# Optimization experiments

Hardware: AMD Instinct MI355X
Metric: run time of the kernel (lower is better)

The kernel has to match this reference:

```python
import jax, jax.numpy as jnp
import numpy as np
import math

B, S, IN, D, H, L, DFF = 8, 512, 32, 512, 8, 6, 2048
DK = D // H
LN_EPS = 1e-5
KL_EPS = 1e-8


def _pos_encoding(seq_len, d_model):
    pe = np.zeros((seq_len, d_model), dtype=np.float32)
    pos = np.arange(seq_len, dtype=np.float32)[:, None]
    div = np.exp(np.arange(0, d_model, 2, dtype=np.float32) * (-math.log(10000.0) / d_model))
    pe[:, 0::2] = np.sin(pos * div)
    pe[:, 1::2] = np.cos(pos * div)
    return jnp.asarray(pe)


def setup_inputs() -> dict:
    key = jax.random.key(0)
    ks = iter(jax.random.split(key, 32))
    g = lambda shape: jax.random.normal(next(ks), shape, dtype=jnp.float32) * 0.02
    return {
        'x': jax.random.normal(next(ks), (B, S, IN), dtype=jnp.float32),
        'W_in': g((IN, D)), 'b_in': jnp.zeros((D,), jnp.float32),
        'pe': _pos_encoding(S, D),
        'Wq': g((L, D, D)), 'Wk': g((L, D, D)), 'Wv': g((L, D, D)),
        'Wo': g((L, D, D)), 'bo': jnp.zeros((L, D), jnp.float32),
        'W1': g((L, D, DFF)), 'b1': jnp.zeros((L, DFF), jnp.float32),
        'W2': g((L, DFF, D)), 'b2': jnp.zeros((L, D), jnp.float32),
        'ln1_g': jnp.ones((L, D), jnp.float32), 'ln1_b': jnp.zeros((L, D), jnp.float32),
        'ln2_g': jnp.ones((L, D), jnp.float32), 'ln2_b': jnp.zeros((L, D), jnp.float32),
        'W_out': g((D, IN)), 'b_out': jnp.zeros((IN,), jnp.float32),
        'Ws1': g((D, D // 2)), 'bs1': jnp.zeros((D // 2,), jnp.float32),
        'Ws2': g((D // 2, 1)), 'bs2': jnp.zeros((1,), jnp.float32),
    }


def _layernorm(v, gamma, beta):
    mu = v.mean(-1, keepdims=True)
    var = ((v - mu) ** 2).mean(-1, keepdims=True)
    return (v - mu) * jax.lax.rsqrt(var + LN_EPS) * gamma + beta


def reference(x, W_in, b_in, pe, Wq, Wk, Wv, Wo, bo, W1, b1, W2, b2,
              ln1_g, ln1_b, ln2_g, ln2_b, W_out, b_out, Ws1, bs1, Ws2, bs2):
    b, s, _ = x.shape
    h = x @ W_in + b_in + pe[None, :s, :]
    total_assoc = jnp.zeros((b, s), x.dtype)
    scale = 1.0 / math.sqrt(DK)
    prior = 1.0 / s + KL_EPS
    for l in range(L):
        # QKV: [b, h, s, dk]
        Q = (h @ Wq[l]).reshape(b, s, H, DK).transpose(0, 2, 1, 3)
        K = (h @ Wk[l]).reshape(b, s, H, DK).transpose(0, 2, 1, 3)
        V = (h @ Wv[l]).reshape(b, s, H, DK).transpose(0, 2, 1, 3)
        scores = jnp.einsum('bhsk,bhtk->bhst', Q, K) * scale
        attn = jax.nn.softmax(scores, axis=-1)  # [b,h,s,s]
        ctx = jnp.einsum('bhst,bhtk->bhsk', attn, V)
        ctx = ctx.transpose(0, 2, 1, 3).reshape(b, s, D)
        attn_out = ctx @ Wo[l] + bo[l]
        # association discrepancy: KL(avg_attn || uniform prior) per query
        avg_attn = attn.mean(axis=1) + KL_EPS  # [b,s,s]
        total_assoc = total_assoc + (avg_attn * jnp.log(avg_attn / prior)).sum(-1)
        h = _layernorm(h + attn_out, ln1_g[l], ln1_b[l])
        ff = jax.nn.relu(h @ W1[l] + b1[l]) @ W2[l] + b2[l]
        h = _layernorm(h + ff, ln2_g[l], ln2_b[l])
    reconstruction = h @ W_out + b_out
    anomaly_scores = jax.nn.sigmoid(jax.nn.relu(h @ Ws1 + bs1) @ Ws2 + bs2)[..., 0]
    avg_association = total_assoc / L
    return reconstruction, anomaly_scores, avg_association
```

## Files before the change

kernel.cpp:

```cpp
#include <hip/hip_runtime.h>
#include <math.h>

typedef __attribute__((ext_vector_type(8))) short bf16x8;
typedef __attribute__((ext_vector_type(4))) float f32x4;

__device__ __forceinline__ short f2bf(float v) {
  union { float f; unsigned u; } x; x.f = v;
  unsigned r = x.u + 0x7fffu + ((x.u >> 16) & 1u);
  return (short)(r >> 16);
}

__device__ __forceinline__ float bf2f(unsigned short u) {
  union { unsigned u; float f; } x; x.u = ((unsigned)u) << 16;
  return x.f;
}

__device__ __forceinline__ void gld_lds16(const void* g, void* l) {
  __builtin_amdgcn_global_load_lds((const __attribute__((address_space(1))) void*)g,
                                   (__attribute__((address_space(3))) void*)l, 16, 0, 0);
}

__global__ __launch_bounds__(256) void transpose_bf(const float* __restrict__ src,
                                                    short* __restrict__ dst,
                                                    int R, int C, size_t sStride, size_t dStride) {
  __shared__ float t[32][33];
  src += blockIdx.z * sStride;
  dst += blockIdx.z * dStride;
  int tx = threadIdx.x & 31, ty = threadIdx.x >> 5;
  int c0 = blockIdx.x * 32, r0 = blockIdx.y * 32;
#pragma unroll
  for (int i = 0; i < 4; i++)
    t[ty + i * 8][tx] = src[(size_t)(r0 + ty + i * 8) * C + c0 + tx];
  __syncthreads();
#pragma unroll
  for (int i = 0; i < 4; i++)
    dst[(size_t)(c0 + ty + i * 8) * R + r0 + tx] = f2bf(t[tx][ty + i * 8]);
}

__global__ void embed_kernel(const float* __restrict__ x, const float* __restrict__ W_in,
                             const float* __restrict__ b_in, const float* __restrict__ pe,
                             float* __restrict__ h, short* __restrict__ hbf) {
  int col = (blockIdx.x & 1) * 256 + threadIdx.x;
  int row = blockIdx.x >> 1;
  int s = row & 511;
  float a = b_in[col] + pe[s * 512 + col];
  const float* xr = x + (size_t)row * 32;
#pragma unroll
  for (int k = 0; k < 32; k++) a += xr[k] * W_in[k * 512 + col];
  h[(size_t)row * 512 + col] = a;
  hbf[(size_t)row * 512 + col] = f2bf(a);
}

template <int EPI, int BM, int BN>
__global__ __launch_bounds__(256) void gemm_bt(const short* __restrict__ A,
                                               const short* __restrict__ Bt,
                                               float* __restrict__ Cf, short* __restrict__ Cb,
                                               const float* __restrict__ bias,
                                               int M, int N, int K) {
  __shared__ short As[BM * 32];
  __shared__ short Bs[BN * 32];
  const int tid = threadIdx.x;
  const int wid = tid >> 6;
  const int lane = tid & 63;
  const int m0 = blockIdx.y * BM;
  const int n0 = blockIdx.x * BN;
  constexpr int WR = BM / 2, WC = BN / 2, FI = WR / 16, FJ = WC / 16;
  const int wr = (wid >> 1) * WR;
  const int wc = (wid & 1) * WC;

  f32x4 acc[FI][FJ];
#pragma unroll
  for (int i = 0; i < FI; i++)
#pragma unroll
    for (int j = 0; j < FJ; j++)
#pragma unroll
      for (int q = 0; q < 4; q++) acc[i][j][q] = 0.0f;

  const short* aBase = A + (size_t)m0 * K;
  const short* bBase = Bt + (size_t)n0 * K;
  const int rowA0 = lane >> 2;
  const int colE = (lane & 3) * 8;
  const int kg = (lane >> 4) * 8;
  const int r16 = lane & 15;
  constexpr int NA = BM / 16, NCALLS = (BM + BN) / 16;

  for (int kt = 0; kt < K; kt += 32) {
    __syncthreads();
#pragma unroll
    for (int c = 0; c < NCALLS / 4; ++c) {
      int s = c * 4 + wid;
      if (s < NA)
        gld_lds16(aBase + (size_t)(s * 16 + rowA0) * K + kt + colE, As + s * 512);
      else
        gld_lds16(bBase + (size_t)((s - NA) * 16 + rowA0) * K + kt + colE, Bs + (s - NA) * 512);
    }
    __syncthreads();
    bf16x8 af[FI], bfr[FJ];
#pragma unroll
    for (int i = 0; i < FI; i++)
      af[i] = *(const bf16x8*)&As[(wr + i * 16 + r16) * 32 + kg];
#pragma unroll
    for (int j = 0; j < FJ; j++)
      bfr[j] = *(const bf16x8*)&Bs[(wc + j * 16 + r16) * 32 + kg];
#pragma unroll
    for (int i = 0; i < FI; i++)
#pragma unroll
      for (int j = 0; j < FJ; j++)
        acc[i][j] = __builtin_amdgcn_mfma_f32_16x16x32_bf16(af[i], bfr[j], acc[i][j], 0, 0, 0);
  }

  const int col16 = lane & 15;
  const int rowg = (lane >> 4) * 4;
#pragma unroll
  for (int i = 0; i < FI; i++) {
    int row = m0 + wr + i * 16 + rowg;
#pragma unroll
    for (int j = 0; j < FJ; j++) {
      int col = n0 + wc + j * 16 + col16;
      float bv = (EPI == 1 || EPI == 2 || EPI == 4) ? bias[col] : 0.0f;
#pragma unroll
      for (int q = 0; q < 4; q++) {
        float v = acc[i][j][q] + bv;
        if (EPI == 2) {
          v = fmaxf(v, 0.0f);
          Cb[(size_t)(row + q) * N + col] = f2bf(v);
        } else if (EPI == 3 || EPI == 4) {
          Cb[(size_t)(row + q) * N + col] = f2bf(v);
        } else {
          Cf[(size_t)(row + q) * N + col] = v;
        }
      }
    }
  }
}

__global__ __launch_bounds__(256) void sm_kernel(const short* __restrict__ qkvh,
                                                 short* __restrict__ P) {
  const int bh = blockIdx.y, b = bh >> 3, h = bh & 7;
  const int q0 = blockIdx.x * 64;
  const int wid = threadIdx.x >> 6, lane = threadIdx.x & 63;
  const int r16 = lane & 15, g = lane >> 4;

  const short* qp = qkvh + (size_t)(b * 512 + q0 + wid * 16 + r16) * 1536 + h * 64 + g * 8;
  const bf16x8 qa0 = *(const bf16x8*)qp;
  const bf16x8 qa1 = *(const bf16x8*)(qp + 32);

  const short* kbase = qkvh + (size_t)(b * 512) * 1536 + 512 + h * 64 + g * 8;

  f32x4 acc[32];
#pragma unroll
  for (int tt = 0; tt < 32; ++tt) {
    const short* kp = kbase + (size_t)(tt * 16 + r16) * 1536;
    bf16x8 kb0 = *(const bf16x8*)kp;
    bf16x8 kb1 = *(const bf16x8*)(kp + 32);
    f32x4 c = {0.f, 0.f, 0.f, 0.f};
    c = __builtin_amdgcn_mfma_f32_16x16x32_bf16(qa0, kb0, c, 0, 0, 0);
    c = __builtin_amdgcn_mfma_f32_16x16x32_bf16(qa1, kb1, c, 0, 0, 0);
    acc[tt] = c;
  }

  float mx[4] = {-1e30f, -1e30f, -1e30f, -1e30f};
#pragma unroll
  for (int tt = 0; tt < 32; ++tt)
#pragma unroll
    for (int r = 0; r < 4; ++r) mx[r] = fmaxf(mx[r], acc[tt][r]);
#pragma unroll
  for (int r = 0; r < 4; ++r)
#pragma unroll
    for (int m = 8; m; m >>= 1) mx[r] = fmaxf(mx[r], __shfl_xor(mx[r], m, 16));

  float sum[4] = {0.f, 0.f, 0.f, 0.f};
#pragma unroll
  for (int tt = 0; tt < 32; ++tt)
#pragma unroll
    for (int r = 0; r < 4; ++r) {
      float e = __expf((acc[tt][r] - mx[r]) * 0.125f);
      sum[r] += e;
      acc[tt][r] = e;
    }
#pragma unroll
  for (int r = 0; r < 4; ++r)
#pragma unroll
    for (int m = 8; m; m >>= 1) sum[r] += __shfl_xor(sum[r], m, 16);
  float inv[4];
#pragma unroll
  for (int r = 0; r < 4; ++r) inv[r] = 1.0f / sum[r];

  short* prow = P + ((size_t)bh * 512 + q0 + wid * 16 + g * 4) * 512 + r16;
#pragma unroll
  for (int r = 0; r < 4; ++r)
#pragma unroll
    for (int tt = 0; tt < 32; ++tt)
      prow[(size_t)r * 512 + tt * 16] = f2bf(acc[tt][r] * inv[r]);
}

__global__ __launch_bounds__(256) void vt_kernel(const short* __restrict__ qkvh,
                                                 short* __restrict__ Vt) {
  __shared__ short t[32][34];
  const int bh = blockIdx.z, b = bh >> 3, h = bh & 7;
  const int t0 = blockIdx.x * 32, d0 = blockIdx.y * 32;
  const int tx = threadIdx.x & 31, ty = threadIdx.x >> 5;
#pragma unroll
  for (int i = 0; i < 4; i++)
    t[ty + i * 8][tx] = qkvh[(size_t)(b * 512 + t0 + ty + i * 8) * 1536 + 1024 + h * 64 + d0 + tx];
  __syncthreads();
#pragma unroll
  for (int i = 0; i < 4; i++)
    Vt[((size_t)bh * 64 + d0 + ty + i * 8) * 512 + t0 + tx] = t[tx][ty + i * 8];
}

__global__ __launch_bounds__(256) void pv_gemm(const short* __restrict__ P,
                                               const short* __restrict__ Vt,
                                               short* __restrict__ ctxb) {
  __shared__ short As[128 * 32];
  __shared__ short Bs[64 * 32];
  const int bh = blockIdx.y, b = bh >> 3, h = bh & 7;
  const int m0 = blockIdx.x * 128;
  const int tid = threadIdx.x, wid = tid >> 6, lane = tid & 63;
  const short* aBase = P + ((size_t)bh * 512 + m0) * 512;
  const short* bBase = Vt + (size_t)bh * 64 * 512;
  const int rowA0 = lane >> 2, colE = (lane & 3) * 8, kg = (lane >> 4) * 8, r16 = lane & 15;

  f32x4 acc[2][4];
#pragma unroll
  for (int i = 0; i < 2; i++)
#pragma unroll
    for (int j = 0; j < 4; j++)
#pragma unroll
      for (int q = 0; q < 4; q++) acc[i][j][q] = 0.0f;

  for (int kt = 0; kt < 512; kt += 32) {
    __syncthreads();
    gld_lds16(aBase + (size_t)(wid * 16 + rowA0) * 512 + kt + colE, As + wid * 512);
    gld_lds16(aBase + (size_t)((wid + 4) * 16 + rowA0) * 512 + kt + colE, As + (wid + 4) * 512);
    gld_lds16(bBase + (size_t)(wid * 16 + rowA0) * 512 + kt + colE, Bs + wid * 512);
    __syncthreads();
    bf16x8 af[2], bfr[4];
#pragma unroll
    for (int i = 0; i < 2; i++)
      af[i] = *(const bf16x8*)&As[(wid * 32 + i * 16 + r16) * 32 + kg];
#pragma unroll
    for (int j = 0; j < 4; j++)
      bfr[j] = *(const bf16x8*)&Bs[(j * 16 + r16) * 32 + kg];
#pragma unroll
    for (int i = 0; i < 2; i++)
#pragma unroll
      for (int j = 0; j < 4; j++)
        acc[i][j] = __builtin_amdgcn_mfma_f32_16x16x32_bf16(af[i], bfr[j], acc[i][j], 0, 0, 0);
  }

  const int rowg = (lane >> 4) * 4;
#pragma unroll
  for (int i = 0; i < 2; i++) {
    int row = m0 + wid * 32 + i * 16 + rowg;
#pragma unroll
    for (int j = 0; j < 4; j++) {
      int col = h * 64 + j * 16 + r16;
#pragma unroll
      for (int q = 0; q < 4; q++)
        ctxb[(size_t)(b * 512 + row + q) * 512 + col] = f2bf(acc[i][j][q]);
    }
  }
}

__global__ __launch_bounds__(256) void kl_kernel(const short* __restrict__ P,
                                                 float* __restrict__ assoc) {
  const int wid = threadIdx.x >> 6, lane = threadIdx.x & 63;
  const int row = blockIdx.x * 4 + wid;
  const int b = row >> 9, q = row & 511;
  const float prior = 1.0f / 512.0f + 1e-8f;
  float hs[8] = {0.f, 0.f, 0.f, 0.f, 0.f, 0.f, 0.f, 0.f};
#pragma unroll
  for (int h = 0; h < 8; ++h) {
    bf16x8 v = *(const bf16x8*)&P[(((size_t)(b * 8 + h)) * 512 + q) * 512 + lane * 8];
#pragma unroll
    for (int k = 0; k < 8; ++k) hs[k] += bf2f((unsigned short)v[k]);
  }
  float s = 0.f;
#pragma unroll
  for (int k = 0; k < 8; ++k) {
    float a = hs[k] * 0.125f + 1e-8f;
    s += a * __logf(a / prior);
  }
#pragma unroll
  for (int m = 32; m; m >>= 1) s += __shfl_xor(s, m, 64);
  if (lane == 0) assoc[row] += s;
}

__global__ __launch_bounds__(256) void ln_kernel(const float* __restrict__ hin,
                                                 const short* __restrict__ res,
                                                 const float* __restrict__ g,
                                                 const float* __restrict__ bta,
                                                 float* __restrict__ hout, short* __restrict__ hbf) {
  const int wid = threadIdx.x >> 6, lane = threadIdx.x & 63;
  const size_t row = (size_t)blockIdx.x * 4 + wid;
  const float* hp = hin + row * 512;
  const short* rp = res + row * 512;
  float v[8], s = 0.f, s2 = 0.f;
#pragma unroll
  for (int i = 0; i < 8; i++) {
    int c = lane + i * 64;
    v[i] = hp[c] + bf2f((unsigned short)rp[c]);
    s += v[i];
    s2 += v[i] * v[i];
  }
#pragma unroll
  for (int m = 32; m; m >>= 1) {
    s += __shfl_xor(s, m, 64);
    s2 += __shfl_xor(s2, m, 64);
  }
  float mu = s * (1.0f / 512.0f);
  float var = s2 * (1.0f / 512.0f) - mu * mu;
  float rs = rsqrtf(var + 1e-5f);
#pragma unroll
  for (int i = 0; i < 8; i++) {
    int c = lane + i * 64;
    float y = (v[i] - mu) * rs * g[c] + bta[c];
    hout[row * 512 + c] = y;
    hbf[row * 512 + c] = f2bf(y);
  }
}

__global__ __launch_bounds__(256) void recon_mfma(const short* __restrict__ hbf,
                                                  const short* __restrict__ WoutT,
                                                  const float* __restrict__ bout,
                                                  float* __restrict__ out) {
  const int wid = threadIdx.x >> 6, lane = threadIdx.x & 63;
  const int r16 = lane & 15, kg = (lane >> 4) * 8;
  const int wbase = blockIdx.x * 128 + wid * 32;

  f32x4 acc[2][2];
#pragma unroll
  for (int i = 0; i < 2; i++)
#pragma unroll
    for (int j = 0; j < 2; j++)
#pragma unroll
      for (int q = 0; q < 4; q++) acc[i][j][q] = 0.0f;

  for (int kt = 0; kt < 512; kt += 32) {
    bf16x8 af[2], bfr[2];
#pragma unroll
    for (int i = 0; i < 2; i++)
      af[i] = *(const bf16x8*)&hbf[(size_t)(wbase + i * 16 + r16) * 512 + kt + kg];
#pragma unroll
    for (int j = 0; j < 2; j++)
      bfr[j] = *(const bf16x8*)&WoutT[(size_t)(j * 16 + r16) * 512 + kt + kg];
#pragma unroll
    for (int i = 0; i < 2; i++)
#pragma unroll
      for (int j = 0; j < 2; j++)
        acc[i][j] = __builtin_amdgcn_mfma_f32_16x16x32_bf16(af[i], bfr[j], acc[i][j], 0, 0, 0);
  }

  const int rowg = (lane >> 4) * 4;
#pragma unroll
  for (int i = 0; i < 2; i++)
#pragma unroll
    for (int j = 0; j < 2; j++) {
      int col = j * 16 + r16;
#pragma unroll
      for (int q = 0; q < 4; q++)
        out[(size_t)(wbase + i * 16 + rowg + q) * 32 + col] = acc[i][j][q] + bout[col];
    }
}

__global__ __launch_bounds__(256) void score2_kernel(const short* __restrict__ s1,
                                                     const float* __restrict__ Ws2,
                                                     const float* __restrict__ bs2,
                                                     float* __restrict__ out) {
  const int wid = threadIdx.x >> 6, lane = threadIdx.x & 63;
  const int row = blockIdx.x * 4 + wid;
  const short* rp = &s1[(size_t)row * 256 + lane * 4];
  float d = 0.f;
#pragma unroll
  for (int e = 0; e < 4; e++) d += bf2f((unsigned short)rp[e]) * Ws2[lane * 4 + e];
#pragma unroll
  for (int m = 32; m; m >>= 1) d += __shfl_xor(d, m, 64);
  if (lane == 0) out[row] = 1.f / (1.f + __expf(-(d + bs2[0])));
}

__global__ void assoc_out_kernel(const float* __restrict__ assoc, float* __restrict__ out) {
  int i = blockIdx.x * 256 + threadIdx.x;
  out[i] = assoc[i] * (1.0f / 6.0f);
}

extern "C" void kernel_launch(void* const* d_in, const int* in_sizes, int n_in,
                              void* d_out, int out_size, void* d_ws, size_t ws_size,
                              hipStream_t stream) {
  const float* x    = (const float*)d_in[0];
  const float* W_in = (const float*)d_in[1];
  const float* b_in = (const float*)d_in[2];
  const float* pe   = (const float*)d_in[3];
  const float* Wq   = (const float*)d_in[4];
  const float* Wk   = (const float*)d_in[5];
  const float* Wv   = (const float*)d_in[6];
  const float* Wo   = (const float*)d_in[7];
  const float* bo   = (const float*)d_in[8];
  const float* W1   = (const float*)d_in[9];
  const float* b1   = (const float*)d_in[10];
  const float* W2   = (const float*)d_in[11];
  const float* b2   = (const float*)d_in[12];
  const float* ln1g = (const float*)d_in[13];
  const float* ln1b = (const float*)d_in[14];
  const float* ln2g = (const float*)d_in[15];
  const float* ln2b = (const float*)d_in[16];
  const float* Wout = (const float*)d_in[17];
  const float* bout = (const float*)d_in[18];
  const float* Ws1  = (const float*)d_in[19];
  const float* bs1  = (const float*)d_in[20];
  const float* Ws2  = (const float*)d_in[21];
  const float* bs2  = (const float*)d_in[22];

  char* p = (char*)d_ws;
  auto alloc = [&](size_t bytes) {
    void* r = (void*)p;
    p += (bytes + 255) & ~(size_t)255;
    return r;
  };
  float* h     = (float*)alloc((size_t)4096 * 512 * 4);
  short* h_bf  = (short*)alloc((size_t)4096 * 512 * 2);
  short* qkvh  = (short*)alloc((size_t)4096 * 1536 * 2);
  short* aout  = (short*)alloc((size_t)4096 * 512 * 2);
  short* ctxb  = (short*)alloc((size_t)4096 * 512 * 2);
  short* ff1b  = (short*)alloc((size_t)4096 * 2048 * 2);
  short* ff2   = (short*)alloc((size_t)4096 * 512 * 2);
  float* assoc = (float*)alloc((size_t)4096 * 4);
  short* Pbuf  = (short*)alloc((size_t)64 * 512 * 512 * 2);
  short* Vt    = (short*)alloc((size_t)64 * 64 * 512 * 2);
  short* sc1   = (short*)alloc((size_t)4096 * 256 * 2);
  short* qkvt  = (short*)alloc((size_t)6 * 1536 * 512 * 2);
  short* wot   = (short*)alloc((size_t)6 * 512 * 512 * 2);
  short* w1t   = (short*)alloc((size_t)6 * 2048 * 512 * 2);
  short* w2t   = (short*)alloc((size_t)6 * 512 * 2048 * 2);
  short* ws1t  = (short*)alloc((size_t)256 * 512 * 2);
  short* woutT = (short*)alloc((size_t)32 * 512 * 2);

  transpose_bf<<<dim3(16, 16, 6), 256, 0, stream>>>(Wq, qkvt, 512, 512, 262144, 786432);
  transpose_bf<<<dim3(16, 16, 6), 256, 0, stream>>>(Wk, qkvt + 262144, 512, 512, 262144, 786432);
  transpose_bf<<<dim3(16, 16, 6), 256, 0, stream>>>(Wv, qkvt + 524288, 512, 512, 262144, 786432);
  transpose_bf<<<dim3(16, 16, 6), 256, 0, stream>>>(Wo, wot, 512, 512, 262144, 262144);
  transpose_bf<<<dim3(64, 16, 6), 256, 0, stream>>>(W1, w1t, 512, 2048, 1048576, 1048576);
  transpose_bf<<<dim3(16, 64, 6), 256, 0, stream>>>(W2, w2t, 2048, 512, 1048576, 1048576);
  transpose_bf<<<dim3(8, 16, 1), 256, 0, stream>>>(Ws1, ws1t, 512, 256, 0, 0);
  transpose_bf<<<dim3(1, 16, 1), 256, 0, stream>>>(Wout, woutT, 512, 32, 0, 0);

  hipMemsetAsync(assoc, 0, 4096 * 4, stream);
  embed_kernel<<<8192, 256, 0, stream>>>(x, W_in, b_in, pe, h, h_bf);

  for (int l = 0; l < 6; ++l) {
    gemm_bt<3, 128, 128><<<dim3(12, 32), 256, 0, stream>>>(h_bf, qkvt + (size_t)l * 786432,
                                                           nullptr, qkvh, nullptr, 4096, 1536, 512);
    vt_kernel<<<dim3(16, 2, 64), 256, 0, stream>>>(qkvh, Vt);
    sm_kernel<<<dim3(8, 64), 256, 0, stream>>>(qkvh, Pbuf);
    pv_gemm<<<dim3(4, 64), 256, 0, stream>>>(Pbuf, Vt, ctxb);
    kl_kernel<<<1024, 256, 0, stream>>>(Pbuf, assoc);
    gemm_bt<4, 64, 64><<<dim3(8, 64), 256, 0, stream>>>(ctxb, wot + (size_t)l * 262144, nullptr,
                                                        aout, bo + l * 512, 4096, 512, 512);
    ln_kernel<<<1024, 256, 0, stream>>>(h, aout, ln1g + l * 512, ln1b + l * 512, h, h_bf);
    gemm_bt<2, 128, 128><<<dim3(16, 32), 256, 0, stream>>>(h_bf, w1t + (size_t)l * 1048576, nullptr,
                                                           ff1b, b1 + l * 2048, 4096, 2048, 512);
    gemm_bt<4, 64, 64><<<dim3(8, 64), 256, 0, stream>>>(ff1b, w2t + (size_t)l * 1048576, nullptr,
                                                        ff2, b2 + l * 512, 4096, 512, 2048);
    ln_kernel<<<1024, 256, 0, stream>>>(h, ff2, ln2g + l * 512, ln2b + l * 512, h, h_bf);
  }

  float* out = (float*)d_out;
  recon_mfma<<<32, 256, 0, stream>>>(h_bf, woutT, bout, out);
  gemm_bt<2, 128, 128><<<dim3(2, 32), 256, 0, stream>>>(h_bf, ws1t, nullptr, sc1, bs1,
                                                        4096, 256, 512);
  score2_kernel<<<1024, 256, 0, stream>>>(sc1, Ws2, bs2, out + 131072);
  assoc_out_kernel<<<16, 256, 0, stream>>>(assoc, out + 131072 + 4096);
}
```

Measured before the change: 899.1 us.

## Deepen GEMM K-tile to 64, enlarge Wo/W2 tiles, merge small launches

Makes the bf16 MFMA GEMM's K-step a template parameter and uses a K-tile of 64 everywhere. This halves the number of barrier pairs and LDS load rounds per output tile. The Wo and FFN2 projections move from 64x64 to 128x64 blocks, which halves their grid size and raises reuse per block. The three QKV weight transposes are merged into one launch, and the association output scaling is folded into the score kernel to remove launches. LDS use per block doubles, which may lower occupancy, and the smaller grids of 256 blocks may underfill the GPU.

```diff
diff --git a/kernel.cpp b/kernel.cpp
--- a/kernel.cpp
+++ b/kernel.cpp
@@ -37,6 +37,26 @@
     dst[(size_t)(c0 + ty + i * 8) * R + r0 + tx] = f2bf(t[tx][ty + i * 8]);
 }
 
+__global__ __launch_bounds__(256) void transpose_qkv(const float* __restrict__ Wq,
+                                                     const float* __restrict__ Wk,
+                                                     const float* __restrict__ Wv,
+                                                     short* __restrict__ qkvt) {
+  __shared__ float t[32][33];
+  const int z = blockIdx.z;
+  const int which = z / 6, l = z % 6;
+  const float* src = (which == 0 ? Wq : which == 1 ? Wk : Wv) + (size_t)l * 262144;
+  short* dst = qkvt + (size_t)l * 786432 + (size_t)which * 262144;
+  int tx = threadIdx.x & 31, ty = threadIdx.x >> 5;
+  int c0 = blockIdx.x * 32, r0 = blockIdx.y * 32;
+#pragma unroll
+  for (int i = 0; i < 4; i++)
+    t[ty + i * 8][tx] = src[(size_t)(r0 + ty + i * 8) * 512 + c0 + tx];
+  __syncthreads();
+#pragma unroll
+  for (int i = 0; i < 4; i++)
+    dst[(size_t)(c0 + ty + i * 8) * 512 + r0 + tx] = f2bf(t[tx][ty + i * 8]);
+}
+
 __global__ void embed_kernel(const float* __restrict__ x, const float* __restrict__ W_in,
                              const float* __restrict__ b_in, const float* __restrict__ pe,
                              float* __restrict__ h, short* __restrict__ hbf) {
@@ -51,20 +71,20 @@
   hbf[(size_t)row * 512 + col] = f2bf(a);
 }
 
-template <int EPI, int BM, int BN>
+template <int EPI, int BM, int BN, int BK>
 __global__ __launch_bounds__(256) void gemm_bt(const short* __restrict__ A,
                                                const short* __restrict__ Bt,
                                                float* __restrict__ Cf, short* __restrict__ Cb,
                                                const float* __restrict__ bias,
                                                int M, int N, int K) {
-  __shared__ short As[BM * 32];
-  __shared__ short Bs[BN * 32];
+  __shared__ short As[BM * BK];
+  __shared__ short Bs[BN * BK];
   const int tid = threadIdx.x;
   const int wid = tid >> 6;
   const int lane = tid & 63;
   const int m0 = blockIdx.y * BM;
   const int n0 = blockIdx.x * BN;
-  constexpr int WR = BM / 2, WC = BN / 2, FI = WR / 16, FJ = WC / 16;
+  constexpr int WR = BM / 2, WC = BN / 2, FI = WR / 16, FJ = WC / 16, KK = BK / 32;
   const int wr = (wid >> 1) * WR;
   const int wc = (wid & 1) * WC;
 
@@ -78,35 +98,43 @@
 
   const short* aBase = A + (size_t)m0 * K;
   const short* bBase = Bt + (size_t)n0 * K;
-  const int rowA0 = lane >> 2;
-  const int colE = (lane & 3) * 8;
+  constexpr int RPC = 512 / BK;
+  constexpr int CA = BM / RPC;
+  constexpr int CT = (BM + BN) / RPC;
+  const int rowL = lane / (64 / RPC);
+  const int colE = (lane % (64 / RPC)) * 8;
   const int kg = (lane >> 4) * 8;
   const int r16 = lane & 15;
-  constexpr int NA = BM / 16, NCALLS = (BM + BN) / 16;
-
-  for (int kt = 0; kt < K; kt += 32) {
+
+  for (int kt = 0; kt < K; kt += BK) {
     __syncthreads();
 #pragma unroll
-    for (int c = 0; c < NCALLS / 4; ++c) {
+    for (int c = 0; c < CT / 4; ++c) {
       int s = c * 4 + wid;
-      if (s < NA)
-        gld_lds16(aBase + (size_t)(s * 16 + rowA0) * K + kt + colE, As + s * 512);
+      if (s < CA)
+        gld_lds16(aBase + (size_t)(s * RPC + rowL) * K + kt + colE, As + s * 512);
       else
-        gld_lds16(bBase + (size_t)((s - NA) * 16 + rowA0) * K + kt + colE, Bs + (s - NA) * 512);
+        gld_lds16(bBase + (size_t)((s - CA) * RPC + rowL) * K + kt + colE, Bs + (s - CA) * 512);
     }
     __syncthreads();
-    bf16x8 af[FI], bfr[FJ];
+    bf16x8 af[FI][KK], bfr[FJ][KK];
 #pragma unroll
     for (int i = 0; i < FI; i++)
-      af[i] = *(const bf16x8*)&As[(wr + i * 16 + r16) * 32 + kg];
+#pragma unroll
+      for (int kk = 0; kk < KK; kk++)
+        af[i][kk] = *(const bf16x8*)&As[(wr + i * 16 + r16) * BK + kk * 32 + kg];
 #pragma unroll
     for (int j = 0; j < FJ; j++)
-      bfr[j] = *(const bf16x8*)&Bs[(wc + j * 16 + r16) * 32 + kg];
-#pragma unroll
-    for (int i = 0; i < FI; i++)
-#pragma unroll
-      for (int j = 0; j < FJ; j++)
-        acc[i][j] = __builtin_amdgcn_mfma_f32_16x16x32_bf16(af[i], bfr[j], acc[i][j], 0, 0, 0);
+#pragma unroll
+      for (int kk = 0; kk < KK; kk++)
+        bfr[j][kk] = *(const bf16x8*)&Bs[(wc + j * 16 + r16) * BK + kk * 32 + kg];
+#pragma unroll
+    for (int kk = 0; kk < KK; kk++)
+#pragma unroll
+      for (int i = 0; i < FI; i++)
+#pragma unroll
+        for (int j = 0; j < FJ; j++)
+          acc[i][j] = __builtin_amdgcn_mfma_f32_16x16x32_bf16(af[i][kk], bfr[j][kk], acc[i][j], 0, 0, 0);
   }
 
   const int col16 = lane & 15;
@@ -367,7 +395,9 @@
 __global__ __launch_bounds__(256) void score2_kernel(const short* __restrict__ s1,
                                                      const float* __restrict__ Ws2,
                                                      const float* __restrict__ bs2,
-                                                     float* __restrict__ out) {
+                                                     const float* __restrict__ assoc,
+                                                     float* __restrict__ outScore,
+                                                     float* __restrict__ outAssoc) {
   const int wid = threadIdx.x >> 6, lane = threadIdx.x & 63;
   const int row = blockIdx.x * 4 + wid;
   const short* rp = &s1[(size_t)row * 256 + lane * 4];
@@ -376,12 +406,10 @@
   for (int e = 0; e < 4; e++) d += bf2f((unsigned short)rp[e]) * Ws2[lane * 4 + e];
 #pragma unroll
   for (int m = 32; m; m >>= 1) d += __shfl_xor(d, m, 64);
-  if (lane == 0) out[row] = 1.f / (1.f + __expf(-(d + bs2[0])));
-}
-
-__global__ void assoc_out_kernel(const float* __restrict__ assoc, float* __restrict__ out) {
-  int i = blockIdx.x * 256 + threadIdx.x;
-  out[i] = assoc[i] * (1.0f / 6.0f);
+  if (lane == 0) {
+    outScore[row] = 1.f / (1.f + __expf(-(d + bs2[0])));
+    outAssoc[row] = assoc[row] * (1.0f / 6.0f);
+  }
 }
 
 extern "C" void kernel_launch(void* const* d_in, const int* in_sizes, int n_in,
@@ -435,9 +463,7 @@
   short* ws1t  = (short*)alloc((size_t)256 * 512 * 2);
   short* woutT = (short*)alloc((size_t)32 * 512 * 2);
 
-  transpose_bf<<<dim3(16, 16, 6), 256, 0, stream>>>(Wq, qkvt, 512, 512, 262144, 786432);
-  transpose_bf<<<dim3(16, 16, 6), 256, 0, stream>>>(Wk, qkvt + 262144, 512, 512, 262144, 786432);
-  transpose_bf<<<dim3(16, 16, 6), 256, 0, stream>>>(Wv, qkvt + 524288, 512, 512, 262144, 786432);
+  transpose_qkv<<<dim3(16, 16, 18), 256, 0, stream>>>(Wq, Wk, Wv, qkvt);
   transpose_bf<<<dim3(16, 16, 6), 256, 0, stream>>>(Wo, wot, 512, 512, 262144, 262144);
   transpose_bf<<<dim3(64, 16, 6), 256, 0, stream>>>(W1, w1t, 512, 2048, 1048576, 1048576);
   transpose_bf<<<dim3(16, 64, 6), 256, 0, stream>>>(W2, w2t, 2048, 512, 1048576, 1048576);
@@ -448,26 +474,26 @@
   embed_kernel<<<8192, 256, 0, stream>>>(x, W_in, b_in, pe, h, h_bf);
 
   for (int l = 0; l < 6; ++l) {
-    gemm_bt<3, 128, 128><<<dim3(12, 32), 256, 0, stream>>>(h_bf, qkvt + (size_t)l * 786432,
-                                                           nullptr, qkvh, nullptr, 4096, 1536, 512);
+    gemm_bt<3, 128, 128, 64><<<dim3(12, 32), 256, 0, stream>>>(
+        h_bf, qkvt + (size_t)l * 786432, nullptr, qkvh, nullptr, 4096, 1536, 512);
     vt_kernel<<<dim3(16, 2, 64), 256, 0, stream>>>(qkvh, Vt);
     sm_kernel<<<dim3(8, 64), 256, 0, stream>>>(qkvh, Pbuf);
     pv_gemm<<<dim3(4, 64), 256, 0, stream>>>(Pbuf, Vt, ctxb);
     kl_kernel<<<1024, 256, 0, stream>>>(Pbuf, assoc);
-    gemm_bt<4, 64, 64><<<dim3(8, 64), 256, 0, stream>>>(ctxb, wot + (size_t)l * 262144, nullptr,
-                                                        aout, bo + l * 512, 4096, 512, 512);
+    gemm_bt<4, 128, 64, 64><<<dim3(8, 32), 256, 0, stream>>>(
+        ctxb, wot + (size_t)l * 262144, nullptr, aout, bo + l * 512, 4096, 512, 512);
     ln_kernel<<<1024, 256, 0, stream>>>(h, aout, ln1g + l * 512, ln1b + l * 512, h, h_bf);
-    gemm_bt<2, 128, 128><<<dim3(16, 32), 256, 0, stream>>>(h_bf, w1t + (size_t)l * 1048576, nullptr,
-                                                           ff1b, b1 + l * 2048, 4096, 2048, 512);
-    gemm_bt<4, 64, 64><<<dim3(8, 64), 256, 0, stream>>>(ff1b, w2t + (size_t)l * 1048576, nullptr,
-                                                        ff2, b2 + l * 512, 4096, 512, 2048);
+    gemm_bt<2, 128, 128, 64><<<dim3(16, 32), 256, 0, stream>>>(
+        h_bf, w1t + (size_t)l * 1048576, nullptr, ff1b, b1 + l * 2048, 4096, 2048, 512);
+    gemm_bt<4, 128, 64, 64><<<dim3(8, 32), 256, 0, stream>>>(
+        ff1b, w2t + (size_t)l * 1048576, nullptr, ff2, b2 + l * 512, 4096, 512, 2048);
     ln_kernel<<<1024, 256, 0, stream>>>(h, ff2, ln2g + l * 512, ln2b + l * 512, h, h_bf);
   }
 
   float* out = (float*)d_out;
   recon_mfma<<<32, 256, 0, stream>>>(h_bf, woutT, bout, out);
-  gemm_bt<2, 128, 128><<<dim3(2, 32), 256, 0, stream>>>(h_bf, ws1t, nullptr, sc1, bs1,
-                                                        4096, 256, 512);
-  score2_kernel<<<1024, 256, 0, stream>>>(sc1, Ws2, bs2, out + 131072);
-  assoc_out_kernel<<<16, 256, 0, stream>>>(assoc, out + 131072 + 4096);
-}
+  gemm_bt<2, 128, 128, 64><<<dim3(2, 32), 256, 0, stream>>>(h_bf, ws1t, nullptr, sc1, bs1,
+                                                            4096, 256, 512);
+  score2_kernel<<<1024, 256, 0, stream>>>(sc1, Ws2, bs2, assoc, out + 131072,
+                                          out + 131072 + 4096);
+}
```

Measured after the change: 989.6 us. 1.1x slower.
